# Kernel tuning notes

Measured on AMD Instinct MI355X. Metric: run time of the kernel, lower is better.

Reference implementation:

```python
import jax, jax.numpy as jnp
import numpy as np

N_EMBD = 1024
HEAD_SIZE = 64
WINDOW = 64
N_GLOBAL = 64
N_RANDOM = 64
B, T = 8, 2048


def setup_inputs() -> dict:
    key = jax.random.key(0)
    kx, kc, kk, kq, kv = jax.random.split(key, 5)
    x = jax.random.normal(kx, (B, T, N_EMBD), dtype=jnp.float32)
    random_cols = jax.random.randint(kc, (T, N_RANDOM), 0, T)
    s = 1.0 / np.sqrt(N_EMBD)
    Wk = jax.random.normal(kk, (HEAD_SIZE, N_EMBD), dtype=jnp.float32) * s
    Wq = jax.random.normal(kq, (HEAD_SIZE, N_EMBD), dtype=jnp.float32) * s
    Wv = jax.random.normal(kv, (HEAD_SIZE, N_EMBD), dtype=jnp.float32) * s
    return {"x": x, "random_cols": random_cols, "Wk": Wk, "Wq": Wq, "Wv": Wv}


def _bigbird_mask(Tlen, random_cols):
    rows = jnp.arange(Tlen)[:, None]
    cols = jnp.arange(Tlen)[None, :]
    causal = rows >= cols
    local = (cols >= rows - WINDOW + 1) & (cols <= rows)
    glob = (rows < N_GLOBAL) | (cols < N_GLOBAL)
    rand = jnp.zeros((Tlen, Tlen), dtype=bool).at[
        jnp.arange(Tlen)[:, None], random_cols].set(True)
    return (local | glob | rand) & causal  # [T, T] bool


def reference(x, random_cols, Wk, Wq, Wv):
    # projections (Linear, no bias): [B,T,C] @ [C,H] -> [B,T,H]
    k = jnp.einsum('btc,hc->bth', x, Wk)
    q = jnp.einsum('btc,hc->bth', x, Wq)
    v = jnp.einsum('btc,hc->bth', x, Wv)
    scale = 1.0 / jnp.sqrt(jnp.asarray(HEAD_SIZE, x.dtype))
    scores = jnp.einsum('bqh,bkh->bqk', q, k) * scale  # [B,T,T]
    mask = _bigbird_mask(x.shape[1], random_cols)
    scores = jnp.where(mask[None, :, :], scores, -jnp.inf)
    weights = jax.nn.softmax(scores, axis=-1)
    out = jnp.einsum('bqk,bkh->bqh', weights, v)  # [B,T,H]
    return out
```

## Files before the change

kernel.cpp:

```cpp
#include <hip/hip_runtime.h>
#include <math.h>

#define T_DIM 2048
#define C_DIM 1024
#define H_DIM 64
#define M_TOTAL 16384
#define NQKV 192

typedef __bf16 bf16x8 __attribute__((ext_vector_type(8)));
typedef float f32x4 __attribute__((ext_vector_type(4)));
typedef float f32x2 __attribute__((ext_vector_type(2)));
typedef unsigned short u16x8 __attribute__((ext_vector_type(8)));

#if __has_builtin(__builtin_amdgcn_fdot2_f32_bf16)
#define HAVE_DOT2 1
typedef __bf16 bf16x2 __attribute__((ext_vector_type(2)));
#else
#define HAVE_DOT2 0
#endif

#if __has_builtin(__builtin_amdgcn_global_load_lds)
#define HAVE_GLL 1
__device__ __forceinline__ void gload_lds16(const unsigned short* g, unsigned short* l) {
    __builtin_amdgcn_global_load_lds(
        (const __attribute__((address_space(1))) unsigned int*)(const void*)g,
        (__attribute__((address_space(3))) unsigned int*)(void*)l,
        16, 0, 0);
}
#else
#define HAVE_GLL 0
#endif

__device__ __forceinline__ unsigned short f2bf(float f) {
    unsigned u = __float_as_uint(f);
    unsigned r = (u + 0x7FFFu + ((u >> 16) & 1u)) >> 16;
    return (unsigned short)r;
}
__device__ __forceinline__ float bf2f(unsigned short u) {
    return __uint_as_float(((unsigned)u) << 16);
}
__device__ __forceinline__ float blo(unsigned u) { return __uint_as_float(u << 16); }
__device__ __forceinline__ float bhi(unsigned u) { return __uint_as_float(u & 0xFFFF0000u); }
__device__ __forceinline__ unsigned pack_bf2(float f0, float f1) {
    unsigned u0 = __float_as_uint(f0) + 0x8000u;
    unsigned u1 = __float_as_uint(f1) + 0x8000u;
    return __builtin_amdgcn_perm(u1, u0, 0x07060302u);
}
__device__ __forceinline__ uint4 cvt8(float4 a, float4 b) {
    return make_uint4(pack_bf2(a.x, a.y), pack_bf2(a.z, a.w),
                      pack_bf2(b.x, b.y), pack_bf2(b.z, b.w));
}

__device__ __forceinline__ float dot8bf(u16x8 a, u16x8 b, float c) {
#if HAVE_DOT2
    bf16x8 av = __builtin_bit_cast(bf16x8, a);
    bf16x8 bv = __builtin_bit_cast(bf16x8, b);
    #pragma unroll
    for (int e = 0; e < 4; ++e) {
        bf16x2 ap = {av[2 * e], av[2 * e + 1]};
        bf16x2 bp = {bv[2 * e], bv[2 * e + 1]};
        c = __builtin_amdgcn_fdot2_f32_bf16(ap, bp, c, false);
    }
#else
    #pragma unroll
    for (int e = 0; e < 8; ++e) c = fmaf(bf2f(a[e]), bf2f(b[e]), c);
#endif
    return c;
}

#if __has_builtin(__builtin_amdgcn_update_dpp)
#define HAVE_DPP 1
template<int CTRL>
__device__ __forceinline__ float dppf(float x) {
    int v = __builtin_amdgcn_update_dpp(0, __builtin_bit_cast(int, x),
                                        CTRL, 0xF, 0xF, true);
    return __builtin_bit_cast(float, v);
}
__device__ __forceinline__ float red8(float p) {
    p += dppf<0xB1>(p);
    p += dppf<0x4E>(p);
    p += dppf<0x141>(p);
    return p;
}
#else
#define HAVE_DPP 0
__device__ __forceinline__ float red8(float p) {
    p += __shfl_xor(p, 1); p += __shfl_xor(p, 2); p += __shfl_xor(p, 4);
    return p;
}
#endif

__global__ __launch_bounds__(256) void wconv_kernel(
    const float* __restrict__ Wk,
    const float* __restrict__ Wq,
    const float* __restrict__ Wv,
    unsigned short* __restrict__ wbf)
{
    int t   = blockIdx.x * 256 + threadIdx.x;
    int g8  = t & 7;
    int kc  = (t >> 3) & 15;
    int row = t >> 7;
    const float* src = (row < 64)  ? Wk + (size_t)row * C_DIM
                     : (row < 128) ? Wq + (size_t)(row - 64) * C_DIM
                                   : Wv + (size_t)(row - 128) * C_DIM;
    int ksrc = kc * 64 + ((g8 * 8) ^ ((row & 7) * 8));
    float4 a = *(const float4*)(src + ksrc);
    float4 b = *(const float4*)(src + ksrc + 4);
    *(uint4*)(wbf + (size_t)row * C_DIM + kc * 64 + g8 * 8) = cvt8(a, b);
}

__global__ __launch_bounds__(256) void compact_kernel(
    const int* __restrict__ rnd,
    int* __restrict__ rjc,
    int* __restrict__ nvalb)
{
    __shared__ unsigned bm_all[4][64];
    const int wv = threadIdx.x >> 6;
    const int ln = threadIdx.x & 63;
    const int i  = blockIdx.x * 4 + wv;
    unsigned* bm = bm_all[wv];

    bm[ln] = 0u;
    int  j2 = rnd[i * 64 + ln];
    bool v2 = (j2 < i - 63) && (j2 >= 64);
    if (v2) {
        unsigned old = atomicOr(&bm[j2 >> 5], 1u << (j2 & 31));
        v2 = ((old >> (j2 & 31)) & 1u) == 0u;
    }
    unsigned long long mbal = __ballot(v2);
    const int nval = __popcll(mbal);
    if (v2) {
        int pos = __popcll(mbal & ((1ull << ln) - 1ull));
        rjc[i * 64 + pos] = j2;
    }
    if (ln >= nval) rjc[i * 64 + ln] = 0;
    if (ln == 0) nvalb[i] = nval;
}

__global__ __launch_bounds__(512) void proj_kernel(
    const float* __restrict__ x,
    const unsigned short* __restrict__ wbf,
    unsigned short* __restrict__ qkv)
{
    __shared__ unsigned short Ab[64 * 64];
    __shared__ unsigned short Bb[192 * 64];

    const int m0 = blockIdx.x * 64;
    const int t  = threadIdx.x;
    const int wv = t >> 6, ln = t & 63;
    const int mfr = ln & 15, kq = ln >> 4;
    const int r0 = (wv & 1) * 32;
    const int c0 = (wv >> 1) * 48;

    const int srow  = t >> 3;
    const int sk8   = (t & 7) * 8;
    const int skoff = sk8 ^ ((srow & 7) * 8);

    const float* gpx = x + (size_t)(m0 + srow) * C_DIM + sk8;
    unsigned short* lpx = &Ab[srow * 64 + skoff];

    const int wrow = wv * 8 + (ln >> 3);
    const unsigned short* wsrc = wbf + (size_t)wrow * C_DIM + (ln & 7) * 8;

    f32x4 acc[2][3] = {};

    float4 ra = *(const float4*)(gpx);
    float4 rb = *(const float4*)(gpx + 4);

    for (int kc = 0; kc < C_DIM; kc += 64) {
        __syncthreads();
        *(uint4*)lpx = cvt8(ra, rb);
#if HAVE_GLL
        #pragma unroll
        for (int s = 0; s < 3; ++s)
            gload_lds16(wsrc + (size_t)s * 64 * C_DIM + kc,
                        &Bb[(s * 64 + wv * 8) * 64]);
#else
        #pragma unroll
        for (int s = 0; s < 3; ++s) {
            uint4 w4 = *(const uint4*)(wsrc + (size_t)s * 64 * C_DIM + kc);
            *(uint4*)&Bb[(s * 64 + wv * 8 + (ln >> 3)) * 64 + (ln & 7) * 8] = w4;
        }
#endif
        if (kc + 64 < C_DIM) {
            ra = *(const float4*)(gpx + kc + 64);
            rb = *(const float4*)(gpx + kc + 68);
        }
        __syncthreads();
        #pragma unroll
        for (int ks = 0; ks < 64; ks += 32) {
            bf16x8 af[2], bf[3];
            #pragma unroll
            for (int a = 0; a < 2; ++a) {
                int row = r0 + a * 16 + mfr;
                af[a] = *(const bf16x8*)&Ab[row * 64 + ((ks + kq * 8) ^ ((row & 7) * 8))];
            }
            #pragma unroll
            for (int b2 = 0; b2 < 3; ++b2) {
                int row = c0 + b2 * 16 + mfr;
                bf[b2] = *(const bf16x8*)&Bb[row * 64 + ((ks + kq * 8) ^ ((row & 7) * 8))];
            }
            #pragma unroll
            for (int a = 0; a < 2; ++a)
                #pragma unroll
                for (int b2 = 0; b2 < 3; ++b2)
                    acc[a][b2] = __builtin_amdgcn_mfma_f32_16x16x32_bf16(
                        af[a], bf[b2], acc[a][b2], 0, 0, 0);
        }
    }

    #pragma unroll
    for (int a = 0; a < 2; ++a)
        #pragma unroll
        for (int b2 = 0; b2 < 3; ++b2)
            #pragma unroll
            for (int r = 0; r < 4; ++r) {
                int row = m0 + r0 + a * 16 + kq * 4 + r;
                int col = c0 + b2 * 16 + mfr;
                qkv[(size_t)row * NQKV + col] = f2bf(acc[a][b2][r]);
            }
}

__global__ __launch_bounds__(1024) void attn_kernel(
    const unsigned short* __restrict__ qkv,
    const int*  __restrict__ rjc,
    const int*  __restrict__ nvalb,
    float* __restrict__ out)
{
    __shared__ unsigned short st[286 * 64];

    const int t  = threadIdx.x;
    const int wv = t >> 6;
    const int ln = t & 63;
    const int b  = blockIdx.x & 7;
    const int qb = blockIdx.x >> 3;
    const int i0 = qb * 16;
    const int i  = i0 + wv;
    const int bi = b * T_DIM + i;

    const unsigned short* kb = qkv + (size_t)b * T_DIM * NQKV;
    const unsigned short* vb = kb + 128;

    const int e8 = (ln & 7) * 8;
    const int gg = ln >> 3;

    const int  nval = nvalb[i];
    const int* rji  = rjc + i * 64;
    int rj8[8];
    #pragma unroll
    for (int u = 0; u < 8; ++u) rj8[u] = rji[u * 8 + gg];
    u16x8 qraw = *(const u16x8*)(qkv + (size_t)bi * NQKV + 64 + e8);

    {
        #pragma unroll
        for (int p = 0; p < 3; ++p) {
            int si = p * 128 + (t >> 3);
            if (si < 286) {
                int tp  = (si < 143) ? si : si - 143;
                int col = (tp < 79) ? max(i0 - 63 + tp, 0) : tp - 79;
                const unsigned short* src =
                    ((si < 143) ? kb : vb) + (size_t)col * NQKV + (t & 7) * 8;
#if HAVE_GLL
                gload_lds16(src, &st[(p * 128 + (wv << 3)) * 64]);
#else
                *(uint4*)&st[si * 64 + (t & 7) * 8] = *(const uint4*)src;
#endif
            }
        }
    }
    __syncthreads();

    const int q = wv;
    float p[24];

    #pragma unroll
    for (int n = 0; n < 16; n += 4) {
        u16x8 kf[4];
        #pragma unroll
        for (int u = 0; u < 4; ++u) {
            int s   = (n + u) * 8 + gg;
            int idx = (s < 64) ? (q + 63 - s) : (s + 15);
            kf[u] = *(const u16x8*)&st[idx * 64 + e8];
        }
        #pragma unroll
        for (int u = 0; u < 4; ++u)
            p[n + u] = red8(dot8bf(kf[u], qraw, 0.f));
    }

    if (nval > 0) {
        u16x8 kr[8];
        #pragma unroll
        for (int u = 0; u < 8; ++u)
            kr[u] = *(const u16x8*)(kb + (size_t)rj8[u] * NQKV + e8);
        #pragma unroll
        for (int u = 0; u < 8; ++u)
            p[16 + u] = red8(dot8bf(kr[u], qraw, 0.f));
    } else {
        #pragma unroll
        for (int u = 0; u < 8; ++u) p[16 + u] = 0.f;
    }

    #pragma unroll
    for (int idx = 0; idx < 8; ++idx) {
        bool v = (idx * 8 + gg) <= i;
        p[idx] = v ? p[idx] * 0.125f : -1e30f;
    }
    #pragma unroll
    for (int idx = 8; idx < 16; ++idx) {
        bool v = ((idx - 8) * 8 + gg) < (i - 63);
        p[idx] = v ? p[idx] * 0.125f : -1e30f;
    }
    #pragma unroll
    for (int idx = 16; idx < 24; ++idx) {
        bool v = ((idx - 16) * 8 + gg) < nval;
        p[idx] = v ? p[idx] * 0.125f : -1e30f;
    }

    float mx = p[0];
    #pragma unroll
    for (int idx = 1; idx < 24; ++idx) mx = fmaxf(mx, p[idx]);
    mx = fmaxf(mx, __shfl_xor(mx, 8));
    mx = fmaxf(mx, __shfl_xor(mx, 16));
    mx = fmaxf(mx, __shfl_xor(mx, 32));

    float sum = 0.f;
    #pragma unroll
    for (int idx = 0; idx < 24; ++idx) {
        p[idx] = __expf(p[idx] - mx);
        sum += p[idx];
    }
    sum += __shfl_xor(sum, 8);
    sum += __shfl_xor(sum, 16);
    sum += __shfl_xor(sum, 32);

    f32x2 acc2[4] = {};
    #pragma unroll
    for (int n = 0; n < 16; n += 4) {
        uint4 vf[4];
        #pragma unroll
        for (int u = 0; u < 4; ++u) {
            int s   = (n + u) * 8 + gg;
            int idx = (s < 64) ? (q + 63 - s) : (s + 15);
            vf[u] = *(const uint4*)&st[(143 + idx) * 64 + e8];
        }
        #pragma unroll
        for (int u = 0; u < 4; ++u) {
            float w = p[n + u];
            f32x2 w2 = {w, w};
            f32x2 p0 = {blo(vf[u].x), bhi(vf[u].x)};
            f32x2 p1 = {blo(vf[u].y), bhi(vf[u].y)};
            f32x2 p2 = {blo(vf[u].z), bhi(vf[u].z)};
            f32x2 p3 = {blo(vf[u].w), bhi(vf[u].w)};
            acc2[0] += w2 * p0;
            acc2[1] += w2 * p1;
            acc2[2] += w2 * p2;
            acc2[3] += w2 * p3;
        }
    }

    if (nval > 0) {
        uint4 vr[8];
        #pragma unroll
        for (int u = 0; u < 8; ++u)
            vr[u] = *(const uint4*)(vb + (size_t)rj8[u] * NQKV + e8);
        #pragma unroll
        for (int u = 0; u < 8; ++u) {
            float w = p[16 + u];
            f32x2 w2 = {w, w};
            f32x2 p0 = {blo(vr[u].x), bhi(vr[u].x)};
            f32x2 p1 = {blo(vr[u].y), bhi(vr[u].y)};
            f32x2 p2 = {blo(vr[u].z), bhi(vr[u].z)};
            f32x2 p3 = {blo(vr[u].w), bhi(vr[u].w)};
            acc2[0] += w2 * p0;
            acc2[1] += w2 * p1;
            acc2[2] += w2 * p2;
            acc2[3] += w2 * p3;
        }
    }

    float acc[8] = { acc2[0][0], acc2[0][1], acc2[1][0], acc2[1][1],
                     acc2[2][0], acc2[2][1], acc2[3][0], acc2[3][1] };
    #pragma unroll
    for (int m = 8; m <= 32; m <<= 1)
        #pragma unroll
        for (int e = 0; e < 8; ++e)
            acc[e] += __shfl_xor(acc[e], m);

    if (ln < 8) {
        float inv = 1.f / sum;
        float* op = &out[(size_t)bi * H_DIM + e8];
        *(float4*)op       = make_float4(acc[0]*inv, acc[1]*inv, acc[2]*inv, acc[3]*inv);
        *(float4*)(op + 4) = make_float4(acc[4]*inv, acc[5]*inv, acc[6]*inv, acc[7]*inv);
    }
}

extern "C" void kernel_launch(void* const* d_in, const int* in_sizes, int n_in,
                              void* d_out, int out_size, void* d_ws, size_t ws_size,
                              hipStream_t stream) {
    const float* x   = (const float*)d_in[0];
    const int*   rnd = (const int*)  d_in[1];
    const float* Wk  = (const float*)d_in[2];
    const float* Wq  = (const float*)d_in[3];
    const float* Wv  = (const float*)d_in[4];
    float* out = (float*)d_out;

    unsigned short* qkv = (unsigned short*)d_ws;
    int* rjc   = (int*)((char*)d_ws + 6291456);
    int* nvalb = rjc + T_DIM * 64;
    unsigned short* wbf = (unsigned short*)((char*)d_ws + 6823936);

    wconv_kernel<<<96, 256, 0, stream>>>(Wk, Wq, Wv, wbf);
    compact_kernel<<<T_DIM / 4, 256, 0, stream>>>(rnd, rjc, nvalb);
    proj_kernel<<<M_TOTAL / 64, 512, 0, stream>>>(x, wbf, qkv);
    attn_kernel<<<M_TOTAL / 16, 1024, 0, stream>>>(qkv, rjc, nvalb, out);
}
```

Before: 146.2 us.

## Compute dense window/global attention with MFMA and a transposed V copy

```diff
diff --git a/kernel.cpp b/kernel.cpp
--- a/kernel.cpp
+++ b/kernel.cpp
@@ -6,6 +6,7 @@
 #define H_DIM 64
 #define M_TOTAL 16384
 #define NQKV 192
+#define VTS 2176
 
 typedef __bf16 bf16x8 __attribute__((ext_vector_type(8)));
 typedef float f32x4 __attribute__((ext_vector_type(4)));
@@ -82,31 +83,73 @@
     p += dppf<0x141>(p);
     return p;
 }
+__device__ __forceinline__ float redsum16(float p) {
+    p += dppf<0xB1>(p);
+    p += dppf<0x4E>(p);
+    p += dppf<0x141>(p);
+    p += dppf<0x140>(p);
+    return p;
+}
+__device__ __forceinline__ float redmax16(float p) {
+    p = fmaxf(p, dppf<0xB1>(p));
+    p = fmaxf(p, dppf<0x4E>(p));
+    p = fmaxf(p, dppf<0x141>(p));
+    p = fmaxf(p, dppf<0x140>(p));
+    return p;
+}
+__device__ __forceinline__ float xor8sum(float p) {
+    return p + dppf<0x140>(p);
+}
+__device__ __forceinline__ float xor8max(float p) {
+    return fmaxf(p, dppf<0x140>(p));
+}
 #else
 #define HAVE_DPP 0
 __device__ __forceinline__ float red8(float p) {
     p += __shfl_xor(p, 1); p += __shfl_xor(p, 2); p += __shfl_xor(p, 4);
     return p;
 }
+__device__ __forceinline__ float redsum16(float p) {
+    p += __shfl_xor(p, 1); p += __shfl_xor(p, 2);
+    p += __shfl_xor(p, 4); p += __shfl_xor(p, 8);
+    return p;
+}
+__device__ __forceinline__ float redmax16(float p) {
+    p = fmaxf(p, __shfl_xor(p, 1)); p = fmaxf(p, __shfl_xor(p, 2));
+    p = fmaxf(p, __shfl_xor(p, 4)); p = fmaxf(p, __shfl_xor(p, 8));
+    return p;
+}
+__device__ __forceinline__ float xor8sum(float p) { return p + __shfl_xor(p, 8); }
+__device__ __forceinline__ float xor8max(float p) { return fmaxf(p, __shfl_xor(p, 8)); }
 #endif
 
 __global__ __launch_bounds__(256) void wconv_kernel(
     const float* __restrict__ Wk,
     const float* __restrict__ Wq,
     const float* __restrict__ Wv,
-    unsigned short* __restrict__ wbf)
+    unsigned short* __restrict__ wbf,
+    unsigned short* __restrict__ vTz)
 {
-    int t   = blockIdx.x * 256 + threadIdx.x;
-    int g8  = t & 7;
-    int kc  = (t >> 3) & 15;
-    int row = t >> 7;
-    const float* src = (row < 64)  ? Wk + (size_t)row * C_DIM
-                     : (row < 128) ? Wq + (size_t)(row - 64) * C_DIM
-                                   : Wv + (size_t)(row - 128) * C_DIM;
-    int ksrc = kc * 64 + ((g8 * 8) ^ ((row & 7) * 8));
-    float4 a = *(const float4*)(src + ksrc);
-    float4 b = *(const float4*)(src + ksrc + 4);
-    *(uint4*)(wbf + (size_t)row * C_DIM + kc * 64 + g8 * 8) = cvt8(a, b);
+    int t = blockIdx.x * 256 + threadIdx.x;
+    if (t < 24576) {
+        int g8  = t & 7;
+        int kc  = (t >> 3) & 15;
+        int row = t >> 7;
+        const float* src = (row < 64)  ? Wk + (size_t)row * C_DIM
+                         : (row < 128) ? Wq + (size_t)(row - 64) * C_DIM
+                                       : Wv + (size_t)(row - 128) * C_DIM;
+        int ksrc = kc * 64 + ((g8 * 8) ^ ((row & 7) * 8));
+        float4 a = *(const float4*)(src + ksrc);
+        float4 b = *(const float4*)(src + ksrc + 4);
+        *(uint4*)(wbf + (size_t)row * C_DIM + kc * 64 + g8 * 8) = cvt8(a, b);
+    } else {
+        int t2    = t - 24576;
+        int rowid = t2 >> 4;
+        int sub   = t2 & 15;
+        int off   = (sub < 8) ? sub * 8 : 2112 + (sub - 8) * 8;
+        uint4 z = make_uint4(0u, 0u, 0u, 0u);
+        *(uint4*)(vTz + (size_t)rowid * VTS + off) = z;
+    }
 }
 
 __global__ __launch_bounds__(256) void compact_kernel(
@@ -140,10 +183,12 @@
 __global__ __launch_bounds__(512) void proj_kernel(
     const float* __restrict__ x,
     const unsigned short* __restrict__ wbf,
-    unsigned short* __restrict__ qkv)
+    unsigned short* __restrict__ qkv,
+    unsigned short* __restrict__ vT)
 {
     __shared__ unsigned short Ab[64 * 64];
     __shared__ unsigned short Bb[192 * 64];
+    __shared__ unsigned short vst[64 * 72];
 
     const int m0 = blockIdx.x * 64;
     const int t  = threadIdx.x;
@@ -219,30 +264,65 @@
                 int col = c0 + b2 * 16 + mfr;
                 qkv[(size_t)row * NQKV + col] = f2bf(acc[a][b2][r]);
             }
+
+    if (wv >= 4) {
+        if (wv < 6) {
+            #pragma unroll
+            for (int a = 0; a < 2; ++a)
+                #pragma unroll
+                for (int r = 0; r < 4; ++r)
+                    vst[mfr * 72 + r0 + a * 16 + kq * 4 + r] = f2bf(acc[a][2][r]);
+        } else {
+            #pragma unroll
+            for (int b2 = 0; b2 < 3; ++b2)
+                #pragma unroll
+                for (int a = 0; a < 2; ++a)
+                    #pragma unroll
+                    for (int r = 0; r < 4; ++r)
+                        vst[(16 + b2 * 16 + mfr) * 72 + r0 + a * 16 + kq * 4 + r]
+                            = f2bf(acc[a][b2][r]);
+        }
+    }
+    __syncthreads();
+    {
+        int h  = t >> 3;
+        int ch = t & 7;
+        uint4 vv = *(const uint4*)&vst[h * 72 + ch * 8];
+        size_t bb = (size_t)(m0 >> 11);
+        int    tt = m0 & 2047;
+        *(uint4*)(vT + (bb * 64 + h) * VTS + 64 + tt + ch * 8) = vv;
+    }
 }
 
 __global__ __launch_bounds__(1024) void attn_kernel(
     const unsigned short* __restrict__ qkv,
+    const unsigned short* __restrict__ vT,
     const int*  __restrict__ rjc,
     const int*  __restrict__ nvalb,
     float* __restrict__ out)
 {
-    __shared__ unsigned short st[286 * 64];
-
-    const int t  = threadIdx.x;
-    const int wv = t >> 6;
-    const int ln = t & 63;
+    __shared__ unsigned short Qst[16 * 72];
+    __shared__ float          sc [16 * 162];
+    __shared__ unsigned short pw [16 * 168];
+    __shared__ float          outR[16 * 72];
+    __shared__ float          invs[16];
+
+    const int tid = threadIdx.x;
+    const int wv = tid >> 6;
+    const int ln = tid & 63;
     const int b  = blockIdx.x & 7;
-    const int qb = blockIdx.x >> 3;
-    const int i0 = qb * 16;
+    const int i0 = (blockIdx.x >> 3) << 4;
     const int i  = i0 + wv;
     const int bi = b * T_DIM + i;
 
-    const unsigned short* kb = qkv + (size_t)b * T_DIM * NQKV;
-    const unsigned short* vb = kb + 128;
-
-    const int e8 = (ln & 7) * 8;
-    const int gg = ln >> 3;
+    const unsigned short* kb  = qkv + (size_t)b * T_DIM * NQKV;
+    const unsigned short* vb  = kb + 128;
+    const unsigned short* vTb = vT + (size_t)b * 64 * VTS + 64;
+
+    const int e8  = (ln & 7) * 8;
+    const int gg  = ln >> 3;
+    const int m15 = ln & 15, kq4 = ln >> 4;
+    const int q   = wv;
 
     const int  nval = nvalb[i];
     const int* rji  = rjc + i * 64;
@@ -251,42 +331,10 @@
     for (int u = 0; u < 8; ++u) rj8[u] = rji[u * 8 + gg];
     u16x8 qraw = *(const u16x8*)(qkv + (size_t)bi * NQKV + 64 + e8);
 
-    {
-        #pragma unroll
-        for (int p = 0; p < 3; ++p) {
-            int si = p * 128 + (t >> 3);
-            if (si < 286) {
-                int tp  = (si < 143) ? si : si - 143;
-                int col = (tp < 79) ? max(i0 - 63 + tp, 0) : tp - 79;
-                const unsigned short* src =
-                    ((si < 143) ? kb : vb) + (size_t)col * NQKV + (t & 7) * 8;
-#if HAVE_GLL
-                gload_lds16(src, &st[(p * 128 + (wv << 3)) * 64]);
-#else
-                *(uint4*)&st[si * 64 + (t & 7) * 8] = *(const uint4*)src;
-#endif
-            }
-        }
-    }
+    if (ln < 8) *(uint4*)&Qst[wv * 72 + ln * 8] = __builtin_bit_cast(uint4, qraw);
     __syncthreads();
 
-    const int q = wv;
-    float p[24];
-
-    #pragma unroll
-    for (int n = 0; n < 16; n += 4) {
-        u16x8 kf[4];
-        #pragma unroll
-        for (int u = 0; u < 4; ++u) {
-            int s   = (n + u) * 8 + gg;
-            int idx = (s < 64) ? (q + 63 - s) : (s + 15);
-            kf[u] = *(const u16x8*)&st[idx * 64 + e8];
-        }
-        #pragma unroll
-        for (int u = 0; u < 4; ++u)
-            p[n + u] = red8(dot8bf(kf[u], qraw, 0.f));
-    }
-
+    float prs[8];
     if (nval > 0) {
         u16x8 kr[8];
         #pragma unroll
@@ -294,70 +342,81 @@
             kr[u] = *(const u16x8*)(kb + (size_t)rj8[u] * NQKV + e8);
         #pragma unroll
         for (int u = 0; u < 8; ++u)
-            p[16 + u] = red8(dot8bf(kr[u], qraw, 0.f));
+            prs[u] = red8(dot8bf(kr[u], qraw, 0.f));
     } else {
         #pragma unroll
-        for (int u = 0; u < 8; ++u) p[16 + u] = 0.f;
-    }
-
-    #pragma unroll
-    for (int idx = 0; idx < 8; ++idx) {
-        bool v = (idx * 8 + gg) <= i;
-        p[idx] = v ? p[idx] * 0.125f : -1e30f;
-    }
-    #pragma unroll
-    for (int idx = 8; idx < 16; ++idx) {
-        bool v = ((idx - 8) * 8 + gg) < (i - 63);
-        p[idx] = v ? p[idx] * 0.125f : -1e30f;
-    }
-    #pragma unroll
-    for (int idx = 16; idx < 24; ++idx) {
-        bool v = ((idx - 16) * 8 + gg) < nval;
-        p[idx] = v ? p[idx] * 0.125f : -1e30f;
-    }
-
-    float mx = p[0];
-    #pragma unroll
-    for (int idx = 1; idx < 24; ++idx) mx = fmaxf(mx, p[idx]);
-    mx = fmaxf(mx, __shfl_xor(mx, 8));
-    mx = fmaxf(mx, __shfl_xor(mx, 16));
-    mx = fmaxf(mx, __shfl_xor(mx, 32));
-
-    float sum = 0.f;
-    #pragma unroll
-    for (int idx = 0; idx < 24; ++idx) {
-        p[idx] = __expf(p[idx] - mx);
-        sum += p[idx];
-    }
-    sum += __shfl_xor(sum, 8);
-    sum += __shfl_xor(sum, 16);
-    sum += __shfl_xor(sum, 32);
+        for (int u = 0; u < 8; ++u) prs[u] = 0.f;
+    }
+
+    if (wv < 9) {
+        int u   = wv * 16 + m15;
+        int col = (u < 64) ? u : max(i0 + u - 128, 0);
+        const unsigned short* kcol = kb + (size_t)col * NQKV;
+        f32x4 c4 = {0.f, 0.f, 0.f, 0.f};
+        #pragma unroll
+        for (int ks = 0; ks < 64; ks += 32) {
+            bf16x8 af = *(const bf16x8*)&Qst[m15 * 72 + ks + kq4 * 8];
+            bf16x8 bf = *(const bf16x8*)(kcol + ks + kq4 * 8);
+            c4 = __builtin_amdgcn_mfma_f32_16x16x32_bf16(af, bf, c4, 0, 0, 0);
+        }
+        #pragma unroll
+        for (int r = 0; r < 4; ++r)
+            sc[(kq4 * 4 + r) * 162 + u] = c4[r];
+    }
+    __syncthreads();
+
+    const float* scq = sc + wv * 162;
+    float s0 = scq[ln];
+    float s1 = scq[64 + ln];
+    float s2 = (ln < 16) ? scq[128 + ln] : 0.f;
+    bool v0 = (ln < i - 63);
+    bool v1 = (ln >= q + 1) && (i0 + ln - 64 >= 0);
+    bool v2 = (ln <= q);
+    s0 = v0 ? s0 * 0.125f : -1e30f;
+    s1 = v1 ? s1 * 0.125f : -1e30f;
+    s2 = v2 ? s2 * 0.125f : -1e30f;
+    #pragma unroll
+    for (int j = 0; j < 8; ++j) {
+        bool vj = (j * 8 + gg) < nval;
+        prs[j] = vj ? prs[j] * 0.125f : -1e30f;
+    }
+
+    float mf = fmaxf(s0, fmaxf(s1, s2));
+    mf = redmax16(mf);
+    mf = fmaxf(mf, __shfl_xor(mf, 16));
+    mf = fmaxf(mf, __shfl_xor(mf, 32));
+    float mr = prs[0];
+    #pragma unroll
+    for (int j = 1; j < 8; ++j) mr = fmaxf(mr, prs[j]);
+    mr = xor8max(mr);
+    mr = fmaxf(mr, __shfl_xor(mr, 16));
+    mr = fmaxf(mr, __shfl_xor(mr, 32));
+    float mx = fmaxf(mf, mr);
+
+    float e0 = v0 ? __expf(s0 - mx) : 0.f;
+    float e1 = v1 ? __expf(s1 - mx) : 0.f;
+    float e2 = v2 ? __expf(s2 - mx) : 0.f;
+    float sumf = e0 + e1 + e2;
+    sumf = redsum16(sumf);
+    sumf += __shfl_xor(sumf, 16);
+    sumf += __shfl_xor(sumf, 32);
+    float er[8], sumr = 0.f;
+    #pragma unroll
+    for (int j = 0; j < 8; ++j) {
+        er[j] = __expf(prs[j] - mx);
+        sumr += er[j];
+    }
+    sumr = xor8sum(sumr);
+    sumr += __shfl_xor(sumr, 16);
+    sumr += __shfl_xor(sumr, 32);
+    float sum = sumf + sumr;
+
+    unsigned short* pwq = pw + wv * 168;
+    pwq[ln]      = f2bf(e0);
+    pwq[64 + ln] = f2bf(e1);
+    if (ln < 32) pwq[128 + ln] = (ln < 16) ? f2bf(e2) : (unsigned short)0;
 
     f32x2 acc2[4] = {};
-    #pragma unroll
-    for (int n = 0; n < 16; n += 4) {
-        uint4 vf[4];
-        #pragma unroll
-        for (int u = 0; u < 4; ++u) {
-            int s   = (n + u) * 8 + gg;
-            int idx = (s < 64) ? (q + 63 - s) : (s + 15);
-            vf[u] = *(const uint4*)&st[(143 + idx) * 64 + e8];
-        }
-        #pragma unroll
-        for (int u = 0; u < 4; ++u) {
-            float w = p[n + u];
-            f32x2 w2 = {w, w};
-            f32x2 p0 = {blo(vf[u].x), bhi(vf[u].x)};
-            f32x2 p1 = {blo(vf[u].y), bhi(vf[u].y)};
-            f32x2 p2 = {blo(vf[u].z), bhi(vf[u].z)};
-            f32x2 p3 = {blo(vf[u].w), bhi(vf[u].w)};
-            acc2[0] += w2 * p0;
-            acc2[1] += w2 * p1;
-            acc2[2] += w2 * p2;
-            acc2[3] += w2 * p3;
-        }
-    }
-
     if (nval > 0) {
         uint4 vr[8];
         #pragma unroll
@@ -365,7 +424,7 @@
             vr[u] = *(const uint4*)(vb + (size_t)rj8[u] * NQKV + e8);
         #pragma unroll
         for (int u = 0; u < 8; ++u) {
-            float w = p[16 + u];
+            float w = er[u];
             f32x2 w2 = {w, w};
             f32x2 p0 = {blo(vr[u].x), bhi(vr[u].x)};
             f32x2 p1 = {blo(vr[u].y), bhi(vr[u].y)};
@@ -377,7 +436,6 @@
             acc2[3] += w2 * p3;
         }
     }
-
     float acc[8] = { acc2[0][0], acc2[0][1], acc2[1][0], acc2[1][1],
                      acc2[2][0], acc2[2][1], acc2[3][0], acc2[3][1] };
     #pragma unroll
@@ -385,12 +443,31 @@
         #pragma unroll
         for (int e = 0; e < 8; ++e)
             acc[e] += __shfl_xor(acc[e], m);
-
     if (ln < 8) {
-        float inv = 1.f / sum;
-        float* op = &out[(size_t)bi * H_DIM + e8];
-        *(float4*)op       = make_float4(acc[0]*inv, acc[1]*inv, acc[2]*inv, acc[3]*inv);
-        *(float4*)(op + 4) = make_float4(acc[4]*inv, acc[5]*inv, acc[6]*inv, acc[7]*inv);
+        *(float4*)&outR[wv * 72 + ln * 8]     = make_float4(acc[0], acc[1], acc[2], acc[3]);
+        *(float4*)&outR[wv * 72 + ln * 8 + 4] = make_float4(acc[4], acc[5], acc[6], acc[7]);
+    }
+    if (ln == 0) invs[wv] = 1.f / sum;
+    __syncthreads();
+
+    if (wv < 4) {
+        const int h = wv * 16 + m15;
+        const unsigned short* vrow = vTb + (size_t)h * VTS;
+        f32x4 c4 = {0.f, 0.f, 0.f, 0.f};
+        #pragma unroll
+        for (int ks = 0; ks < 160; ks += 32) {
+            int u0 = ks + kq4 * 8;
+            int cb = (u0 < 64) ? u0 : (i0 + u0 - 128);
+            bf16x8 bf = *(const bf16x8*)(vrow + cb);
+            bf16x8 af = *(const bf16x8*)&pw[m15 * 168 + u0];
+            c4 = __builtin_amdgcn_mfma_f32_16x16x32_bf16(af, bf, c4, 0, 0, 0);
+        }
+        #pragma unroll
+        for (int r = 0; r < 4; ++r) {
+            int qq = kq4 * 4 + r;
+            float o = (c4[r] + outR[qq * 72 + h]) * invs[qq];
+            out[((size_t)b * T_DIM + i0 + qq) * H_DIM + h] = o;
+        }
     }
 }
 
@@ -408,9 +485,10 @@
     int* rjc   = (int*)((char*)d_ws + 6291456);
     int* nvalb = rjc + T_DIM * 64;
     unsigned short* wbf = (unsigned short*)((char*)d_ws + 6823936);
-
-    wconv_kernel<<<96, 256, 0, stream>>>(Wk, Wq, Wv, wbf);
+    unsigned short* vT  = (unsigned short*)((char*)d_ws + 7217152);
+
+    wconv_kernel<<<128, 256, 0, stream>>>(Wk, Wq, Wv, wbf, vT);
     compact_kernel<<<T_DIM / 4, 256, 0, stream>>>(rnd, rjc, nvalb);
-    proj_kernel<<<M_TOTAL / 64, 512, 0, stream>>>(x, wbf, qkv);
-    attn_kernel<<<M_TOTAL / 16, 1024, 0, stream>>>(qkv, rjc, nvalb, out);
-}
+    proj_kernel<<<M_TOTAL / 64, 512, 0, stream>>>(x, wbf, qkv, vT);
+    attn_kernel<<<M_TOTAL / 16, 1024, 0, stream>>>(qkv, vT, rjc, nvalb, out);
+}
```

Result: faster. 141.9 us (-2.9%).
